# Optimization experiments

Measured on AMD Instinct MI355X. Metric: run time of the kernel, lower is better.

The kernel has to match this reference:

```python
import jax, jax.numpy as jnp
import numpy as np

B, N, DIM = 2, 4096, 1024
HEADS, DH, W = 16, 64, 512
INNER = int(DIM * 2 * 4 / 3)  # 2730 (GEGLU FeedForward, mult=4)


def setup_inputs() -> dict:
    key = jax.random.key(0)
    ks = jax.random.split(key, 6)
    rn = lambda k, shape, sc: jax.random.normal(k, shape, jnp.float32) * sc
    return {
        "x": rn(ks[0], (B, N, DIM), 1.0),
        "ln1_w": jnp.ones((DIM,), jnp.float32),
        "ln1_b": jnp.zeros((DIM,), jnp.float32),
        "w_qkv": rn(ks[1], (DIM, 3 * HEADS * DH), 0.02),
        "w_out": rn(ks[2], (HEADS * DH, DIM), 0.02),
        "ln2_w": jnp.ones((DIM,), jnp.float32),
        "w_ff1": rn(ks[3], (DIM, 2 * INNER), 0.02),
        "w_ff2": rn(ks[4], (INNER, DIM), 0.02),
    }


def _layernorm(x, w, b=None, eps=1e-5):
    m = x.mean(-1, keepdims=True)
    v = x.var(-1, keepdims=True)
    y = (x - m) * jax.lax.rsqrt(v + eps) * w
    return y + b if b is not None else y


def _rotary_freqs(n, d):
    inv = 1.0 / (10000.0 ** (jnp.arange(0, d, 2, dtype=jnp.float32) / d))
    f = jnp.arange(n, dtype=jnp.float32)[:, None] * inv[None, :]  # [n, d/2]
    return jnp.concatenate([f, f], axis=-1)  # [n, d]


def _rotate_half(x):
    x1, x2 = jnp.split(x, 2, axis=-1)
    return jnp.concatenate([-x2, x1], axis=-1)


def _apply_rotary(x, freqs):
    return x * jnp.cos(freqs) + _rotate_half(x) * jnp.sin(freqs)


def reference(x, ln1_w, ln1_b, w_qkv, w_out, ln2_w, w_ff1, w_ff2):
    # ---- LocalMHA (prenorm, causal windowed attention, look_backward=1) ----
    h = _layernorm(x, ln1_w, ln1_b)
    qkv = h @ w_qkv  # [b, n, 3*h*d]
    q, k, v = jnp.split(qkv, 3, axis=-1)
    to_heads = lambda t: t.reshape(B, N, HEADS, DH).transpose(0, 2, 1, 3)  # [b,h,n,d]
    q, k, v = map(to_heads, (q, k, v))

    freqs = _rotary_freqs(N, DH)  # [n, d]
    q = _apply_rotary(q, freqs)
    k = _apply_rotary(k, freqs)
    q = q * (DH ** -0.5)

    nw = N // W
    bq = q.reshape(B, HEADS, nw, W, DH)
    bk = k.reshape(B, HEADS, nw, W, DH)
    bv = v.reshape(B, HEADS, nw, W, DH)

    def look_back(t):  # prepend previous window (zeros for first window)
        prev = jnp.concatenate([jnp.zeros_like(t[:, :, :1]), t[:, :, :-1]], axis=2)
        return jnp.concatenate([prev, t], axis=3)  # [b,h,nw,2w,d]

    kk, vv = look_back(bk), look_back(bv)

    tq = jnp.arange(N).reshape(nw, W)
    tprev = jnp.concatenate([jnp.full((1, W), -1, tq.dtype), tq[:-1]], axis=0)
    tk = jnp.concatenate([tprev, tq], axis=1)  # [nw, 2w]
    mask = (tq[:, :, None] >= tk[:, None, :]) & (tk[:, None, :] >= 0)  # causal + pad

    sim = jnp.einsum('bhnqd,bhnkd->bhnqk', bq, kk)
    sim = jnp.where(mask, sim, jnp.finfo(sim.dtype).min / 2)
    attn = jax.nn.softmax(sim, axis=-1)
    o = jnp.einsum('bhnqk,bhnkd->bhnqd', attn, vv)
    o = o.reshape(B, HEADS, N, DH).transpose(0, 2, 1, 3).reshape(B, N, HEADS * DH)
    x = o @ w_out + x  # residual

    # ---- FeedForward: LN(gamma only) -> GEGLU -> Linear, residual ----
    h = _layernorm(x, ln2_w)
    u = h @ w_ff1
    a, g = jnp.split(u, 2, axis=-1)
    x = (a * jax.nn.gelu(g, approximate=False)) @ w_ff2 + x
    return x
```

## Files before the change

kernel.cpp:

```cpp
#include <hip/hip_runtime.h>
#include <stdint.h>

typedef unsigned short u16;
typedef unsigned int u32;

#define BATCH 2
#define NSEQ  4096
#define DIM   1024
#define HEADS 16
#define DH    64
#define WIN   512
#define INNER 2730
#define ROWS  8192
#define QKV_N 3072
#define FF1_N 5460
#define FF1_NP 5504
#define INNER_P 2752
#define KROT 0.28782313663f

typedef __attribute__((ext_vector_type(8))) short short8;
typedef __attribute__((ext_vector_type(4))) float float4v;

__device__ __forceinline__ float bf2f(u16 u){ union{u32 i;float f;}c; c.i=((u32)u)<<16; return c.f; }
__device__ __forceinline__ u16 f2bf(float f){ union{float f;u32 i;}c; c.f=f; u32 i=c.i;
    return (u16)((i + 0x7FFFu + ((i>>16)&1u))>>16); }

__device__ __forceinline__ float gelu_fast(float g) {
    float t = 0.7978845608f * (g + 0.044715f * g * g * g);
    float th = 1.f - 2.f / (1.f + __expf(2.f * t));
    return 0.5f * g * (1.f + th);
}

__device__ __forceinline__ void gl_lds16(const u16* g, const u16* ldsbase) {
    __builtin_amdgcn_global_load_lds(
        (const __attribute__((address_space(1))) u32*)(uintptr_t)g,
        (__attribute__((address_space(3))) u32*)(uintptr_t)ldsbase,
        16, 0, 0);
}

__device__ __forceinline__ int ff1_src(int n, bool& ok) {
    int t = n >> 7, m = n & 127, j = m >> 4, l = m & 15;
    int p = t * 64 + ((j >> 1) << 4) + l;
    ok = (p < INNER);
    return (j & 1) ? (INNER + p) : p;
}

template <bool REMAP>
__global__ __launch_bounds__(256) void wtrans_kernel(const float* __restrict__ w, u16* __restrict__ wt,
                                                     int K0, int N0, int K1, int N1) {
    __shared__ float tile[32][33];
    int kt = blockIdx.x, nt = blockIdx.y;
    int tx = threadIdx.x & 31, ty = threadIdx.x >> 5;
    int nl = nt * 32 + tx;
    bool ok = (nl < N1);
    int sc = nl;
    if (REMAP) { bool v; sc = ff1_src(nl < N1 ? nl : 0, v); ok = ok && v; }
    else ok = ok && (nl < N0);
#pragma unroll
    for (int yy = 0; yy < 4; yy++) {
        int k = kt*32 + ty + yy*8;
        tile[ty+yy*8][tx] = (k < K0 && ok) ? w[(size_t)k*N0 + sc] : 0.f;
    }
    __syncthreads();
#pragma unroll
    for (int yy = 0; yy < 4; yy++) {
        int n = nt*32 + ty + yy*8, k = kt*32 + tx;
        if (n < N1 && k < K1) wt[(size_t)n*K1 + k] = f2bf(tile[tx][ty+yy*8]);
    }
}

__global__ __launch_bounds__(256) void ln_kernel(const float* __restrict__ x,
                                                 const float* __restrict__ w,
                                                 const float* __restrict__ b,
                                                 u16* __restrict__ out) {
    int row = blockIdx.x;
    const float* xr = x + (size_t)row * DIM;
    int t = threadIdx.x;
    float v[4];
    float s = 0.f, s2 = 0.f;
#pragma unroll
    for (int i = 0; i < 4; i++) {
        float f = xr[t + 256 * i];
        v[i] = f; s += f; s2 += f * f;
    }
#pragma unroll
    for (int off = 32; off; off >>= 1) { s += __shfl_xor(s, off); s2 += __shfl_xor(s2, off); }
    __shared__ float ls[10];
    int wave = t >> 6, lane = t & 63;
    if (lane == 0) { ls[wave] = s; ls[4 + wave] = s2; }
    __syncthreads();
    if (t == 0) {
        float ts  = ls[0] + ls[1] + ls[2] + ls[3];
        float ts2 = ls[4] + ls[5] + ls[6] + ls[7];
        float mean = ts * (1.f / DIM);
        float var  = ts2 * (1.f / DIM) - mean * mean;
        ls[8] = mean; ls[9] = 1.f / sqrtf(var + 1e-5f);
    }
    __syncthreads();
    float mean = ls[8], inv = ls[9];
    u16* orow = out + (size_t)row * DIM;
#pragma unroll
    for (int i = 0; i < 4; i++) {
        int c = t + 256 * i;
        float y = (v[i] - mean) * inv * w[c];
        if (b) y += b[c];
        orow[c] = f2bf(y);
    }
}

template <int MODE>
__global__ __launch_bounds__(256) void gemm_tile(const u16* __restrict__ A,
                                                 const u16* __restrict__ Bt,
                                                 const float* __restrict__ resid,
                                                 void* __restrict__ Cv,
                                                 int M, int N, int K) {
    __shared__ u16 As[2][128 * 32];
    __shared__ u16 Bs[2][128 * 32];
    int tiles_n = N >> 7;
    int gs  = tiles_n << 3;
    int gid = blockIdx.x / gs;
    int loc = blockIdx.x % gs;
    int tm = gid * 8 + (loc & 7);
    int tn = loc >> 3;
    int tid = threadIdx.x, wave = tid >> 6, lane = tid & 63;
    int quad = lane >> 4, l15 = lane & 15;
    int wm = wave >> 1, wn = wave & 1;
    int srow = wave * 32 + (lane >> 2);
    int sgrp = (lane & 3) ^ ((srow >> 1) & 3);
    const u16* Ag = A  + (size_t)(tm * 128 + srow) * K + sgrp * 8;
    const u16* Bg = Bt + (size_t)(tn * 128 + srow) * K + sgrp * 8;
    const u16* Alb0 = &As[0][wave * 1024];
    const u16* Blb0 = &Bs[0][wave * 1024];
    const u16* Alb1 = &As[1][wave * 1024];
    const u16* Blb1 = &Bs[1][wave * 1024];
    int rg = (l15 >> 1) & 3;
    float4v acc[4][4];
#pragma unroll
    for (int i = 0; i < 4; i++)
#pragma unroll
        for (int j = 0; j < 4; j++) acc[i][j] = (float4v){0.f, 0.f, 0.f, 0.f};

    gl_lds16(Ag,                Alb0);
    gl_lds16(Ag + (size_t)16*K, Alb0 + 512);
    gl_lds16(Bg,                Blb0);
    gl_lds16(Bg + (size_t)16*K, Blb0 + 512);
    __syncthreads();

    int nk = K >> 5;
    for (int t = 0; t < nk; ++t) {
        int buf = t & 1;
        if (t + 1 < nk) {
            int k0 = (t + 1) << 5;
            const u16* Al = buf ? Alb0 : Alb1;
            const u16* Bl = buf ? Blb0 : Blb1;
            gl_lds16(Ag + k0,                Al);
            gl_lds16(Ag + (size_t)16*K + k0, Al + 512);
            gl_lds16(Bg + k0,                Bl);
            gl_lds16(Bg + (size_t)16*K + k0, Bl + 512);
        }
        const u16* Asb = &As[buf][0];
        const u16* Bsb = &Bs[buf][0];
        short8 af[4], bf[4];
#pragma unroll
        for (int i = 0; i < 4; i++)
            af[i] = *(const short8*)&Asb[(wm*64 + i*16 + l15)*32 + ((quad ^ rg) * 8)];
#pragma unroll
        for (int j = 0; j < 4; j++)
            bf[j] = *(const short8*)&Bsb[(wn*64 + j*16 + l15)*32 + ((quad ^ rg) * 8)];
#pragma unroll
        for (int i = 0; i < 4; i++)
#pragma unroll
            for (int j = 0; j < 4; j++)
                acc[i][j] = __builtin_amdgcn_mfma_f32_16x16x32_bf16(af[i], bf[j], acc[i][j], 0, 0, 0);
        __syncthreads();
    }
    if (MODE == 3) {
        u16* ag = (u16*)Cv;
#pragma unroll
        for (int i = 0; i < 4; i++) {
#pragma unroll
            for (int r = 0; r < 4; r++) {
                size_t row = (size_t)(tm*128 + wm*64 + i*16 + quad*4 + r);
#pragma unroll
                for (int jp = 0; jp < 2; jp++) {
                    float a = acc[i][2*jp][r];
                    float g = acc[i][2*jp+1][r];
                    int col = tn*64 + wn*32 + jp*16 + l15;
                    ag[row * INNER_P + col] = f2bf(a * gelu_fast(g));
                }
            }
        }
        return;
    }
    if (MODE == 2) {
        u16* C = (u16*)Cv;
        int sector = tn >> 3;
        if (sector < 2) {
            float inv0 = __expf(-(float)l15 * KROT);
            float inv1 = __expf(-(float)(l15 + 16) * KROT);
            float sc = (sector == 0) ? 0.125f : 1.0f;
#pragma unroll
            for (int i = 0; i < 4; i++) {
#pragma unroll
                for (int r = 0; r < 4; r++) {
                    int row = tm*128 + wm*64 + i*16 + quad*4 + r;
                    float fn = (float)(row & (NSEQ - 1));
                    float s0, c0, s1, c1;
                    __sincosf(fn * inv0, &s0, &c0);
                    __sincosf(fn * inv1, &s1, &c1);
                    float a0 = acc[i][0][r], a1 = acc[i][1][r];
                    float a2 = acc[i][2][r], a3 = acc[i][3][r];
                    size_t base = (size_t)row * N + tn*128 + wn*64 + l15;
                    C[base]      = f2bf((a0*c0 - a2*s0) * sc);
                    C[base + 16] = f2bf((a1*c1 - a3*s1) * sc);
                    C[base + 32] = f2bf((a2*c0 + a0*s0) * sc);
                    C[base + 48] = f2bf((a3*c1 + a1*s1) * sc);
                }
            }
        } else {
#pragma unroll
            for (int i = 0; i < 4; i++)
#pragma unroll
                for (int r = 0; r < 4; r++) {
                    size_t base = (size_t)(tm*128 + wm*64 + i*16 + quad*4 + r) * N + tn*128 + wn*64 + l15;
#pragma unroll
                    for (int j = 0; j < 4; j++) C[base + j*16] = f2bf(acc[i][j][r]);
                }
        }
        return;
    }
#pragma unroll
    for (int i = 0; i < 4; i++) {
#pragma unroll
        for (int r = 0; r < 4; r++) {
            size_t row = (size_t)(tm*128 + wm*64 + i*16 + quad*4 + r);
#pragma unroll
            for (int j = 0; j < 4; j++) {
                int col = tn*128 + wn*64 + j*16 + l15;
                size_t idx = row * N + col;
                float v = acc[i][j][r];
                if (MODE == 1) { if (resid) v += resid[idx]; ((float*)Cv)[idx] = v; }
                else ((u16*)Cv)[idx] = f2bf(v);
            }
        }
    }
}

__global__ __launch_bounds__(256) void vtrans_kernel(const u16* __restrict__ qkv, u16* __restrict__ vt) {
    __shared__ u16 tile[64][72];
    int t = threadIdx.x;
    int n0 = (blockIdx.x & 63) * 64;
    int hh = (blockIdx.x >> 6) & 15;
    int b  = blockIdx.x >> 10;
    int r = t >> 2, cb = (t & 3) * 16;
    const u16* src = qkv + (size_t)(b * NSEQ + n0 + r) * QKV_N + 2 * DIM + hh * 64 + cb;
    uint4 v0 = *(const uint4*)(src);
    uint4 v1 = *(const uint4*)(src + 8);
    *(uint4*)&tile[r][cb]     = v0;
    *(uint4*)&tile[r][cb + 8] = v1;
    __syncthreads();
    int d = t >> 2, nb = (t & 3) * 16;
    __align__(16) u16 vals[16];
#pragma unroll
    for (int e = 0; e < 16; e++) vals[e] = tile[nb + e][d];
    u16* dst = vt + ((size_t)(b * HEADS + hh) * DH + d) * NSEQ + n0 + nb;
    *(uint4*)(dst)     = *(uint4*)&vals[0];
    *(uint4*)(dst + 8) = *(uint4*)&vals[8];
}

__global__ __launch_bounds__(256) void attn_kernel(const u16* __restrict__ qkv,
                                                   const u16* __restrict__ vt,
                                                   u16* __restrict__ o) {
    __shared__ u16 Ks[128 * 64];
    __shared__ u16 Vs[64 * 128];
    __shared__ u16 p_lds[4][16][136];
    int tid = threadIdx.x, wave = tid >> 6, lane = tid & 63;
    int quad = lane >> 4, l15 = lane & 15;
    int bi = blockIdx.x;
    int qb = bi & 7, w0 = (bi >> 3) & 7, hh = (bi >> 6) & 15, b = bi >> 10;
    int qt = qb * 4 + wave;
    int qlocal = qt * 16 + l15;
    const u16* qp = qkv + (size_t)(b*NSEQ + w0*WIN + qt*16 + l15) * QKV_N + hh*64 + quad*8;
    short8 bq0 = *(const short8*)(qp);
    short8 bq1 = *(const short8*)(qp + 32);
    int krow0 = b * NSEQ + (w0 - 1) * WIN;
    const u16* vbase = vt + (size_t)(b * HEADS + hh) * DH * NSEQ + (w0 - 1) * WIN;
    int ks_row = lane >> 3;
    int ks_g   = (lane & 7) ^ ks_row;
    int vs_row = lane >> 4;
    int vs_j0  = lane & 15;
    int swz = l15 & 7;
    float m_ = -1e30f, l_ = 0.f;
    float4v O[4] = {{0,0,0,0},{0,0,0,0},{0,0,0,0},{0,0,0,0}};
    int cstart = (w0 == 0) ? 4 : 0;
    int clast  = (512 + qb * 64 + 63) >> 7;
    u16 (*pt)[136] = p_lds[wave];
    for (int c = cstart; c <= clast; c++) {
        int kb = c * 128;
        __syncthreads();
#pragma unroll
        for (int i = 0; i < 4; i++) {
            int kloc = wave * 32 + i * 8 + ks_row;
            gl_lds16(qkv + (size_t)(krow0 + kb + kloc) * QKV_N + DIM + hh*64 + ks_g*8,
                     &Ks[(wave*32 + i*8) * 64]);
        }
#pragma unroll
        for (int i = 0; i < 4; i++) {
            int dloc = wave * 16 + i * 4 + vs_row;
            int jsrc = vs_j0 ^ (dloc & 7);
            gl_lds16(vbase + (size_t)dloc * NSEQ + kb + jsrc * 8,
                     &Vs[(wave*16 + i*4) * 128]);
        }
        __syncthreads();
        float4v s[8];
#pragma unroll
        for (int t = 0; t < 8; t++) {
            int krow = (t*16 + l15) * 64;
            short8 ka0 = *(const short8*)&Ks[krow + ((quad    ) ^ swz) * 8];
            short8 ka1 = *(const short8*)&Ks[krow + ((quad + 4) ^ swz) * 8];
            float4v st = {0.f, 0.f, 0.f, 0.f};
            st = __builtin_amdgcn_mfma_f32_16x16x32_bf16(ka0, bq0, st, 0, 0, 0);
            st = __builtin_amdgcn_mfma_f32_16x16x32_bf16(ka1, bq1, st, 0, 0, 0);
            int ck = kb + t*16 + quad*4;
#pragma unroll
            for (int r = 0; r < 4; r++)
                if (ck + r >= 512 && ck + r - 512 > qlocal) st[r] = -1e30f;
            s[t] = st;
        }
        float mc = -1e30f;
#pragma unroll
        for (int t = 0; t < 8; t++)
#pragma unroll
            for (int r = 0; r < 4; r++) mc = fmaxf(mc, s[t][r]);
        mc = fmaxf(mc, __shfl_xor(mc, 16));
        mc = fmaxf(mc, __shfl_xor(mc, 32));
        float mn = fmaxf(m_, mc);
        float alpha = __expf(m_ - mn);
        m_ = mn;
        float su = 0.f;
#pragma unroll
        for (int t = 0; t < 8; t++) {
            union { u16 h[4]; uint2 v; } pk;
#pragma unroll
            for (int r = 0; r < 4; r++) {
                float p = __expf(s[t][r] - mn);
                su += p;
                pk.h[r] = f2bf(p);
            }
            *(uint2*)&pt[l15][t*16 + quad*4] = pk.v;
        }
        su += __shfl_xor(su, 16);
        su += __shfl_xor(su, 32);
        l_ = l_ * alpha + su;
#pragma unroll
        for (int t = 0; t < 4; t++)
#pragma unroll
            for (int r = 0; r < 4; r++) O[t][r] *= alpha;
#pragma unroll
        for (int g = 0; g < 4; g++) {
            short8 pf = *(const short8*)&pt[l15][g*32 + quad*8];
#pragma unroll
            for (int t = 0; t < 4; t++) {
                short8 vf = *(const short8*)&Vs[(t*16 + l15) * 128 + ((g*4 + quad) ^ swz) * 8];
                O[t] = __builtin_amdgcn_mfma_f32_16x16x32_bf16(vf, pf, O[t], 0, 0, 0);
            }
        }
    }
    float inv = 1.f / l_;
    u16* op = o + (size_t)(b*NSEQ + w0*WIN + qt*16 + l15) * DIM + hh*64;
#pragma unroll
    for (int t = 0; t < 4; t++) {
        union { u16 h[4]; uint2 v; } pk;
#pragma unroll
        for (int r = 0; r < 4; r++) pk.h[r] = f2bf(O[t][r] * inv);
        *(uint2*)(op + t*16 + quad*4) = pk.v;
    }
}

extern "C" void kernel_launch(void* const* d_in, const int* in_sizes, int n_in,
                              void* d_out, int out_size, void* d_ws, size_t ws_size,
                              hipStream_t stream) {
    const float* x      = (const float*)d_in[0];
    const float* ln1_w  = (const float*)d_in[1];
    const float* ln1_b  = (const float*)d_in[2];
    const float* w_qkv  = (const float*)d_in[3];
    const float* w_out  = (const float*)d_in[4];
    const float* ln2_w  = (const float*)d_in[5];
    const float* w_ff1  = (const float*)d_in[6];
    const float* w_ff2  = (const float*)d_in[7];
    float* out = (float*)d_out;

    char* ws = (char*)d_ws;
    size_t off = 0;
    auto alloc = [&](size_t bytes) { size_t o = off; off += (bytes + 255) & ~(size_t)255; return o; };
    size_t off_wqt  = alloc((size_t)QKV_N  * DIM * 2);
    size_t off_wot  = alloc((size_t)DIM    * DIM * 2);
    size_t off_wf1t = alloc((size_t)FF1_NP * DIM * 2);
    size_t off_wf2t = alloc((size_t)DIM    * INNER_P * 2);
    size_t off_h    = alloc((size_t)ROWS * DIM * 2);
    size_t sz_qkv = (size_t)ROWS * QKV_N * 2;
    size_t sz_vt  = (size_t)BATCH * HEADS * DH * NSEQ * 2;
    size_t off_qkv  = alloc(sz_qkv);
    size_t off_vt   = alloc(sz_vt);
    size_t off_o    = alloc((size_t)ROWS * DIM * 2);
    size_t off_x1   = alloc((size_t)ROWS * DIM * 4);
    size_t off_ag   = alloc((size_t)ROWS * INNER_P * 2);

    u16* wqt  = (u16*)(ws + off_wqt);
    u16* wot  = (u16*)(ws + off_wot);
    u16* wf1t = (u16*)(ws + off_wf1t);
    u16* wf2t = (u16*)(ws + off_wf2t);
    u16* h    = (u16*)(ws + off_h);
    u16* qkv  = (u16*)(ws + off_qkv);
    u16* vt   = (u16*)(ws + off_vt);
    u16* o    = (u16*)(ws + off_o);
    float* x1 = (float*)(ws + off_x1);
    u16* ag   = (u16*)(ws + off_ag);

    wtrans_kernel<false><<<dim3(32, 96),  256, 0, stream>>>(w_qkv, wqt,  DIM,   QKV_N, DIM,     QKV_N);
    wtrans_kernel<false><<<dim3(32, 32),  256, 0, stream>>>(w_out, wot,  DIM,   DIM,   DIM,     DIM);
    wtrans_kernel<true ><<<dim3(32, 172), 256, 0, stream>>>(w_ff1, wf1t, DIM,   FF1_N, DIM,     FF1_NP);
    wtrans_kernel<false><<<dim3(86, 32),  256, 0, stream>>>(w_ff2, wf2t, INNER, DIM,   INNER_P, DIM);

    ln_kernel<<<ROWS, 256, 0, stream>>>(x, ln1_w, ln1_b, h);
    gemm_tile<2><<<(ROWS/128) * (QKV_N/128), 256, 0, stream>>>(h, wqt, nullptr, qkv, ROWS, QKV_N, DIM);
    vtrans_kernel<<<BATCH * HEADS * (NSEQ / 64), 256, 0, stream>>>(qkv, vt);
    attn_kernel<<<BATCH * HEADS * 8 * 8, 256, 0, stream>>>(qkv, vt, o);
    gemm_tile<1><<<(ROWS/128) * (DIM/128), 256, 0, stream>>>(o, wot, x, x1, ROWS, DIM, DIM);
    ln_kernel<<<ROWS, 256, 0, stream>>>(x1, ln2_w, nullptr, h);
    gemm_tile<3><<<(ROWS/128) * (FF1_NP/128), 256, 0, stream>>>(h, wf1t, nullptr, ag, ROWS, FF1_NP, DIM);
    gemm_tile<1><<<(ROWS/128) * (DIM/128), 256, 0, stream>>>(ag, wf2t, x1, out, ROWS, DIM, INNER_P);

    (void)in_sizes; (void)n_in; (void)out_size; (void)ws_size;
}
```

Before: 544.1 us.

## Add 256x256-tile 4-stage pipelined GEMM for QKV and FF1 projections

Adds a new GEMM kernel with 256x256 output tiles, 512 threads, and a 4-deep LDS ring of async global-to-LDS loads with explicit vmcnt waits and MFMA priority hints. It is used for the QKV (rotary epilogue) and FF1 (GEGLU epilogue) projections. The larger tiles raise data reuse per loaded byte, and the deeper prefetch hides memory latency. FF1/INNER padding grows to multiples of 256, which adds some wasted compute. Using 128KB of dynamic LDS limits blocks per CU.

```diff
diff --git a/kernel.cpp b/kernel.cpp
--- a/kernel.cpp
+++ b/kernel.cpp
@@ -14,8 +14,8 @@
 #define ROWS  8192
 #define QKV_N 3072
 #define FF1_N 5460
-#define FF1_NP 5504
-#define INNER_P 2752
+#define FF1_NP 5632
+#define INNER_P 2816
 #define KROT 0.28782313663f
 
 typedef __attribute__((ext_vector_type(8))) short short8;
@@ -105,6 +105,138 @@
         float y = (v[i] - mean) * inv * w[c];
         if (b) y += b[c];
         orow[c] = f2bf(y);
+    }
+}
+
+template <int MODE>
+__global__ __launch_bounds__(512, 2) void gemm256(const u16* __restrict__ A,
+                                                  const u16* __restrict__ Bt,
+                                                  void* __restrict__ Cv,
+                                                  int N, int K) {
+    extern __shared__ u16 lds[];
+    u16* Asm = lds;
+    u16* Bsm = lds + 4 * 8192;
+    int tiles_n = N >> 8;
+    int gs  = tiles_n << 3;
+    int gid = blockIdx.x / gs;
+    int loc = blockIdx.x % gs;
+    int tm = gid * 8 + (loc & 7);
+    int tn = loc >> 3;
+    int tid = threadIdx.x, wave = tid >> 6, lane = tid & 63;
+    int quad = lane >> 4, l15 = lane & 15;
+    int wm = wave >> 2, wn = wave & 3;
+    int srow = wave * 16 + (lane >> 2);
+    int sgrp = (lane & 3) ^ ((srow >> 1) & 3);
+    const u16* Ag = A  + (size_t)(tm * 256 + srow) * K + sgrp * 8;
+    const u16* Bg = Bt + (size_t)(tn * 256 + srow) * K + sgrp * 8;
+    u16* Asw = Asm + wave * 512;
+    u16* Bsw = Bsm + wave * 512;
+    int rg = (l15 >> 1) & 3;
+    int nk = K >> 5;
+
+    float4v acc[8][4];
+#pragma unroll
+    for (int i = 0; i < 8; i++)
+#pragma unroll
+        for (int j = 0; j < 4; j++) acc[i][j] = (float4v){0.f, 0.f, 0.f, 0.f};
+
+    auto stage = [&](int t) {
+        int b = t & 3;
+        int k0 = t << 5;
+        gl_lds16(Ag + k0,                   Asw + b * 8192);
+        gl_lds16(Ag + (size_t)128 * K + k0, Asw + b * 8192 + 4096);
+        gl_lds16(Bg + k0,                   Bsw + b * 8192);
+        gl_lds16(Bg + (size_t)128 * K + k0, Bsw + b * 8192 + 4096);
+    };
+    auto compute = [&](int t) {
+        const u16* Ab = Asm + (t & 3) * 8192;
+        const u16* Bb = Bsm + (t & 3) * 8192;
+        short8 af[8], bfr[4];
+#pragma unroll
+        for (int i = 0; i < 8; i++)
+            af[i] = *(const short8*)&Ab[(wm*128 + i*16 + l15) * 32 + ((quad ^ rg) * 8)];
+#pragma unroll
+        for (int j = 0; j < 4; j++)
+            bfr[j] = *(const short8*)&Bb[(wn*64 + j*16 + l15) * 32 + ((quad ^ rg) * 8)];
+        __builtin_amdgcn_s_setprio(1);
+#pragma unroll
+        for (int i = 0; i < 8; i++)
+#pragma unroll
+            for (int j = 0; j < 4; j++)
+                acc[i][j] = __builtin_amdgcn_mfma_f32_16x16x32_bf16(af[i], bfr[j], acc[i][j], 0, 0, 0);
+        __builtin_amdgcn_s_setprio(0);
+    };
+
+    stage(0); stage(1); stage(2);
+
+#define KSTEP(T, VM) \
+    asm volatile("s_waitcnt vmcnt(" #VM ")" ::: "memory"); \
+    __builtin_amdgcn_s_barrier(); \
+    __builtin_amdgcn_sched_barrier(0); \
+    compute(T); \
+    if ((T) + 3 < nk) stage((T) + 3);
+
+    for (int t = 0; t < nk - 2; ++t) { KSTEP(t, 8); }
+    { KSTEP(nk - 2, 4); }
+    { KSTEP(nk - 1, 0); }
+#undef KSTEP
+
+    if (MODE == 2) {
+        u16* C = (u16*)Cv;
+        int sector = tn >> 2;
+        if (sector < 2) {
+            float inv0 = __expf(-(float)l15 * KROT);
+            float inv1 = __expf(-(float)(l15 + 16) * KROT);
+            float sc = (sector == 0) ? 0.125f : 1.0f;
+#pragma unroll
+            for (int i = 0; i < 8; i++) {
+#pragma unroll
+                for (int r = 0; r < 4; r++) {
+                    int row = tm*256 + wm*128 + i*16 + quad*4 + r;
+                    float fn = (float)(row & (NSEQ - 1));
+                    float s0, c0, s1, c1;
+                    __sincosf(fn * inv0, &s0, &c0);
+                    __sincosf(fn * inv1, &s1, &c1);
+                    float a0 = acc[i][0][r], a1 = acc[i][1][r];
+                    float a2 = acc[i][2][r], a3 = acc[i][3][r];
+                    size_t base = (size_t)row * N + tn*256 + wn*64 + l15;
+                    C[base]      = f2bf((a0*c0 - a2*s0) * sc);
+                    C[base + 16] = f2bf((a1*c1 - a3*s1) * sc);
+                    C[base + 32] = f2bf((a2*c0 + a0*s0) * sc);
+                    C[base + 48] = f2bf((a3*c1 + a1*s1) * sc);
+                }
+            }
+        } else {
+#pragma unroll
+            for (int i = 0; i < 8; i++)
+#pragma unroll
+                for (int r = 0; r < 4; r++) {
+                    size_t base = (size_t)(tm*256 + wm*128 + i*16 + quad*4 + r) * N + tn*256 + wn*64 + l15;
+#pragma unroll
+                    for (int j = 0; j < 4; j++) C[base + j*16] = f2bf(acc[i][j][r]);
+                }
+        }
+        return;
+    }
+    if (MODE == 3) {
+        u16* ag = (u16*)Cv;
+        int t128 = tn * 2 + (wn >> 1);
+        int cb = t128 * 64 + (wn & 1) * 32;
+#pragma unroll
+        for (int i = 0; i < 8; i++) {
+#pragma unroll
+            for (int r = 0; r < 4; r++) {
+                size_t row = (size_t)(tm*256 + wm*128 + i*16 + quad*4 + r);
+#pragma unroll
+                for (int jp = 0; jp < 2; jp++) {
+                    float a = acc[i][2*jp][r];
+                    float g = acc[i][2*jp+1][r];
+                    int col = cb + jp*16 + l15;
+                    ag[row * INNER_P + col] = f2bf(a * gelu_fast(g));
+                }
+            }
+        }
+        return;
     }
 }
 
@@ -173,61 +305,6 @@
             for (int j = 0; j < 4; j++)
                 acc[i][j] = __builtin_amdgcn_mfma_f32_16x16x32_bf16(af[i], bf[j], acc[i][j], 0, 0, 0);
         __syncthreads();
-    }
-    if (MODE == 3) {
-        u16* ag = (u16*)Cv;
-#pragma unroll
-        for (int i = 0; i < 4; i++) {
-#pragma unroll
-            for (int r = 0; r < 4; r++) {
-                size_t row = (size_t)(tm*128 + wm*64 + i*16 + quad*4 + r);
-#pragma unroll
-                for (int jp = 0; jp < 2; jp++) {
-                    float a = acc[i][2*jp][r];
-                    float g = acc[i][2*jp+1][r];
-                    int col = tn*64 + wn*32 + jp*16 + l15;
-                    ag[row * INNER_P + col] = f2bf(a * gelu_fast(g));
-                }
-            }
-        }
-        return;
-    }
-    if (MODE == 2) {
-        u16* C = (u16*)Cv;
-        int sector = tn >> 3;
-        if (sector < 2) {
-            float inv0 = __expf(-(float)l15 * KROT);
-            float inv1 = __expf(-(float)(l15 + 16) * KROT);
-            float sc = (sector == 0) ? 0.125f : 1.0f;
-#pragma unroll
-            for (int i = 0; i < 4; i++) {
-#pragma unroll
-                for (int r = 0; r < 4; r++) {
-                    int row = tm*128 + wm*64 + i*16 + quad*4 + r;
-                    float fn = (float)(row & (NSEQ - 1));
-                    float s0, c0, s1, c1;
-                    __sincosf(fn * inv0, &s0, &c0);
-                    __sincosf(fn * inv1, &s1, &c1);
-                    float a0 = acc[i][0][r], a1 = acc[i][1][r];
-                    float a2 = acc[i][2][r], a3 = acc[i][3][r];
-                    size_t base = (size_t)row * N + tn*128 + wn*64 + l15;
-                    C[base]      = f2bf((a0*c0 - a2*s0) * sc);
-                    C[base + 16] = f2bf((a1*c1 - a3*s1) * sc);
-                    C[base + 32] = f2bf((a2*c0 + a0*s0) * sc);
-                    C[base + 48] = f2bf((a3*c1 + a1*s1) * sc);
-                }
-            }
-        } else {
-#pragma unroll
-            for (int i = 0; i < 4; i++)
-#pragma unroll
-                for (int r = 0; r < 4; r++) {
-                    size_t base = (size_t)(tm*128 + wm*64 + i*16 + quad*4 + r) * N + tn*128 + wn*64 + l15;
-#pragma unroll
-                    for (int j = 0; j < 4; j++) C[base + j*16] = f2bf(acc[i][j][r]);
-                }
-        }
-        return;
     }
 #pragma unroll
     for (int i = 0; i < 4; i++) {
@@ -390,6 +467,13 @@
     const float* w_ff2  = (const float*)d_in[7];
     float* out = (float*)d_out;
 
+    static bool cfg = false;
+    if (!cfg) {
+        hipFuncSetAttribute((const void*)gemm256<2>, hipFuncAttributeMaxDynamicSharedMemorySize, 131072);
+        hipFuncSetAttribute((const void*)gemm256<3>, hipFuncAttributeMaxDynamicSharedMemorySize, 131072);
+        cfg = true;
+    }
+
     char* ws = (char*)d_ws;
     size_t off = 0;
     auto alloc = [&](size_t bytes) { size_t o = off; off += (bytes + 255) & ~(size_t)255; return o; };
@@ -419,16 +503,16 @@
 
     wtrans_kernel<false><<<dim3(32, 96),  256, 0, stream>>>(w_qkv, wqt,  DIM,   QKV_N, DIM,     QKV_N);
     wtrans_kernel<false><<<dim3(32, 32),  256, 0, stream>>>(w_out, wot,  DIM,   DIM,   DIM,     DIM);
-    wtrans_kernel<true ><<<dim3(32, 172), 256, 0, stream>>>(w_ff1, wf1t, DIM,   FF1_N, DIM,     FF1_NP);
-    wtrans_kernel<false><<<dim3(86, 32),  256, 0, stream>>>(w_ff2, wf2t, INNER, DIM,   INNER_P, DIM);
+    wtrans_kernel<true ><<<dim3(32, 176), 256, 0, stream>>>(w_ff1, wf1t, DIM,   FF1_N, DIM,     FF1_NP);
+    wtrans_kernel<false><<<dim3(88, 32),  256, 0, stream>>>(w_ff2, wf2t, INNER, DIM,   INNER_P, DIM);
 
     ln_kernel<<<ROWS, 256, 0, stream>>>(x, ln1_w, ln1_b, h);
-    gemm_tile<2><<<(ROWS/128) * (QKV_N/128), 256, 0, stream>>>(h, wqt, nullptr, qkv, ROWS, QKV_N, DIM);
+    gemm256<2><<<(ROWS/256) * (QKV_N/256), 512, 131072, stream>>>(h, wqt, qkv, QKV_N, DIM);
     vtrans_kernel<<<BATCH * HEADS * (NSEQ / 64), 256, 0, stream>>>(qkv, vt);
     attn_kernel<<<BATCH * HEADS * 8 * 8, 256, 0, stream>>>(qkv, vt, o);
     gemm_tile<1><<<(ROWS/128) * (DIM/128), 256, 0, stream>>>(o, wot, x, x1, ROWS, DIM, DIM);
     ln_kernel<<<ROWS, 256, 0, stream>>>(x1, ln2_w, nullptr, h);
-    gemm_tile<3><<<(ROWS/128) * (FF1_NP/128), 256, 0, stream>>>(h, wf1t, nullptr, ag, ROWS, FF1_NP, DIM);
+    gemm256<3><<<(ROWS/256) * (FF1_NP/256), 512, 131072, stream>>>(h, wf1t, ag, FF1_NP, DIM);
     gemm_tile<1><<<(ROWS/128) * (DIM/128), 256, 0, stream>>>(ag, wf2t, x1, out, ROWS, DIM, INNER_P);
 
     (void)in_sizes; (void)n_in; (void)out_size; (void)ws_size;
```

Result: no change. 537.7 us (-1.2%).
